# Kernel optimization log

Hardware: AMD Instinct MI355X
Metric: run time of the kernel (lower is better)

Reference implementation:

```python
import jax, jax.numpy as jnp
import numpy as np

C, H, W = 128, 128, 128
N_LINES = 8192
N_POINTS = 32
POOL = 4
DIM_FC = 1024


def setup_inputs() -> dict:
    key = jax.random.key(0)
    ks = jax.random.split(key, 8)
    feats = jax.random.normal(ks[0], (C, H, W), dtype=jnp.float32)
    # line endpoints (x1,y1,x2,y2) in feature-map pixel coords
    lines = jax.random.uniform(ks[1], (N_LINES, 4), dtype=jnp.float32) * (H - 1)
    d_in = C * (N_POINTS // POOL)  # 1024
    W1 = jax.random.normal(ks[2], (DIM_FC, d_in), dtype=jnp.float32) * 0.02
    b1 = jax.random.normal(ks[3], (DIM_FC,), dtype=jnp.float32) * 0.02
    W2 = jax.random.normal(ks[4], (DIM_FC, DIM_FC), dtype=jnp.float32) * 0.02
    b2 = jax.random.normal(ks[5], (DIM_FC,), dtype=jnp.float32) * 0.02
    W3 = jax.random.normal(ks[6], (4, DIM_FC), dtype=jnp.float32) * 0.02
    b3 = jax.random.normal(ks[7], (4,), dtype=jnp.float32) * 0.02
    return {
        "features_per_image": feats,
        "lines_per_im": lines,
        "W1": W1, "b1": b1, "W2": W2, "b2": b2, "W3": W3, "b3": b3,
        "n_points": N_POINTS,
        "pool_stride": POOL,
    }


def _extract_pt_feats(features, lines, n_points):
    # features: [C, H, W]; lines: [N, 4]
    c, h, w = features.shape
    tspan = jnp.linspace(0.0, 1.0, n_points).astype(features.dtype)  # [P]
    U, V = lines[:, :2], lines[:, 2:]
    # [N, 2, P] -> interpolate endpoints, shift by 0.5 (torch pixel-center convention)
    pts = U[:, :, None] * tspan + V[:, :, None] * (1.0 - tspan) - 0.5
    pts = pts.transpose(0, 2, 1).reshape(-1, 2)  # [N*P, 2]
    px, py = pts[:, 0], pts[:, 1]
    # NOTE: faithful to torch source: px indexes the h-axis but is clamped with w-1,
    # py indexes the w-axis but is clamped with h-1 (harmless here since H == W).
    px0 = jnp.clip(jnp.floor(px), 0.0, w - 1)
    py0 = jnp.clip(jnp.floor(py), 0.0, h - 1)
    px1 = jnp.clip(px0 + 1.0, 0.0, w - 1)
    py1 = jnp.clip(py0 + 1.0, 0.0, h - 1)
    px0i, py0i = px0.astype(jnp.int32), py0.astype(jnp.int32)
    px1i, py1i = px1.astype(jnp.int32), py1.astype(jnp.int32)
    # four irregular gathers + bilinear weights, fused expression. each term: [C, N*P]
    xp = (features[:, px0i, py0i] * ((py1 - py) * (px1 - px))
          + features[:, px0i, py1i] * ((py - py0) * (px1 - px))
          + features[:, px1i, py0i] * ((py1 - py) * (px - px0))
          + features[:, px1i, py1i] * ((py - py0) * (px - px0)))
    return xp.reshape(c, -1, n_points).transpose(1, 0, 2)  # [N, C, P]


def reference(features_per_image, lines_per_im, W1, b1, W2, b2, W3, b3,
              n_points, pool_stride):
    xp = _extract_pt_feats(features_per_image, lines_per_im, n_points)  # [N, C, P]
    n, c, p = xp.shape
    # MaxPool1d(kernel=stride=pool_stride)
    pooled = xp.reshape(n, c, p // pool_stride, pool_stride).max(axis=-1)
    flat = pooled.reshape(n, -1)  # [N, C*(P//s)]
    h1 = jax.nn.relu(flat @ W1.T + b1)
    h2 = jax.nn.relu(h1 @ W2.T + b2)
    return h2 @ W3.T + b3  # [N, 4]
```

## Files before the change

### kernel.cpp

```cpp
#include <hip/hip_runtime.h>
#include <hip/hip_bf16.h>
#include <cstdint>

typedef __attribute__((ext_vector_type(4))) float f32x4;
typedef __attribute__((ext_vector_type(8))) short short8;

#define DEVI __device__ __forceinline__

DEVI uint16_t f2bf(float v) {
    union { float f; uint32_t u; } c; c.f = v;
    uint32_t u = c.u + 0x7FFFu + ((c.u >> 16) & 1u);
    return (uint16_t)(u >> 16);
}
DEVI float bflo(uint32_t u) { union { uint32_t u; float f; } c; c.u = u << 16; return c.f; }
DEVI float bfhi(uint32_t u) { union { uint32_t u; float f; } c; c.u = u & 0xFFFF0000u; return c.f; }

DEVI void async16(const uint16_t* g, uint16_t* l) {
    __builtin_amdgcn_global_load_lds((const __attribute__((address_space(1))) void*)g,
                                     (__attribute__((address_space(3))) void*)l, 16, 0, 0);
}

__global__ __launch_bounds__(256) void init_out(float* __restrict__ out, const float* __restrict__ b3) {
    const int i = blockIdx.x * 256 + threadIdx.x;
    float4 b = { b3[0], b3[1], b3[2], b3[3] };
    ((float4*)out)[i] = b;
}

__global__ __launch_bounds__(256) void prep_all(const float* __restrict__ f, uint16_t* __restrict__ featT,
                                                const float* __restrict__ W1, uint16_t* __restrict__ W1b,
                                                const float* __restrict__ W2, uint16_t* __restrict__ W2b) {
    if (blockIdx.x < 128) {
        __shared__ uint16_t s[128 * 130];
        const int x = blockIdx.x;
        const float* fx = f + x * 128;
        for (int i = threadIdx.x; i < 16384; i += 256) {
            int c = i >> 7, y = i & 127;
            s[y * 130 + c] = f2bf(fx[c * 16384 + y]);
        }
        __syncthreads();
        uint16_t* o = featT + x * 16384;
        for (int i = threadIdx.x; i < 16384; i += 256) {
            int y = i >> 7, c = i & 127;
            o[i] = s[y * 130 + c];
        }
    } else {
        const int i = (blockIdx.x - 128) * 256 + threadIdx.x;
        float4 a = ((const float4*)W1)[i];
        float4 b = ((const float4*)W2)[i];
        ushort4 pa = { f2bf(a.x), f2bf(a.y), f2bf(a.z), f2bf(a.w) };
        ushort4 pb = { f2bf(b.x), f2bf(b.y), f2bf(b.z), f2bf(b.w) };
        ((ushort4*)W1b)[i] = pa;
        ((ushort4*)W2b)[i] = pb;
    }
}

__global__ __launch_bounds__(256) void extract_k(const float4* __restrict__ lines,
                                                 const uint16_t* __restrict__ featT,
                                                 uint16_t* __restrict__ flat) {
    const int n = blockIdx.x;
    const int tid = threadIdx.x;
    const int lane = tid & 63, wave = tid >> 6;
    const float4 ln = lines[n];
    __shared__ uint16_t ps[1024];
    const uint16_t* fb = featT + lane * 2;

    for (int g2 = 0; g2 < 2; ++g2) {
        const int g = wave * 2 + g2;
        float m0 = -1e30f, m1 = -1e30f;
#pragma unroll
        for (int pp = 0; pp < 4; ++pp) {
            const float t = (float)(g * 4 + pp) * (1.0f / 31.0f);
            const float x = ln.x * t + ln.z * (1.0f - t) - 0.5f;
            const float y = ln.y * t + ln.w * (1.0f - t) - 0.5f;
            const float x0f = fminf(fmaxf(floorf(x), 0.0f), 127.0f);
            const float y0f = fminf(fmaxf(floorf(y), 0.0f), 127.0f);
            const float x1f = fminf(x0f + 1.0f, 127.0f);
            const float y1f = fminf(y0f + 1.0f, 127.0f);
            const int x0 = (int)x0f, x1 = (int)x1f, y0 = (int)y0f, y1 = (int)y1f;
            const float wx1 = x - x0f, wx0 = x1f - x;
            const float wy1 = y - y0f, wy0 = y1f - y;
            const uint32_t u00 = *(const uint32_t*)(fb + ((x0 * 128 + y0) << 7));
            const uint32_t u01 = *(const uint32_t*)(fb + ((x0 * 128 + y1) << 7));
            const uint32_t u10 = *(const uint32_t*)(fb + ((x1 * 128 + y0) << 7));
            const uint32_t u11 = *(const uint32_t*)(fb + ((x1 * 128 + y1) << 7));
            const float w00 = wy0 * wx0, w01 = wy1 * wx0, w10 = wy0 * wx1, w11 = wy1 * wx1;
            const float a = bflo(u00) * w00 + bflo(u01) * w01 + bflo(u10) * w10 + bflo(u11) * w11;
            const float b = bfhi(u00) * w00 + bfhi(u01) * w01 + bfhi(u10) * w10 + bfhi(u11) * w11;
            m0 = fmaxf(m0, a);
            m1 = fmaxf(m1, b);
        }
        ps[lane * 16 + g]     = f2bf(m0);
        ps[lane * 16 + 8 + g] = f2bf(m1);
    }
    __syncthreads();
    *(uint2*)(flat + (size_t)n * 1024 + tid * 4) = ((const uint2*)ps)[tid];
}

template <int FUSE3>
__global__ __launch_bounds__(256) void gemm_bt(const uint16_t* __restrict__ A,
                                               const uint16_t* __restrict__ B,
                                               const float* __restrict__ bias,
                                               uint16_t* __restrict__ Co,
                                               const float* __restrict__ W3,
                                               float* __restrict__ out3,
                                               int M, int N, int K) {
    __shared__ uint16_t As[128 * 64];
    __shared__ uint16_t Bs[128 * 64];
    const int tid = threadIdx.x;
    const int lane = tid & 63, wave = tid >> 6;
    const int nbm = M >> 7;
    const int bm = blockIdx.x % nbm;
    const int bn = blockIdx.x / nbm;
    const int wr = wave >> 1, wc = wave & 1;
    const int l15 = lane & 15, l16 = lane >> 4;

    f32x4 acc[4][4] = {};

    const uint16_t* Ag = A + (size_t)(bm * 128) * K;
    const uint16_t* Bg = B + (size_t)(bn * 128) * K;

    for (int kt = 0; kt < K; kt += 64) {
        if (kt) __syncthreads();
#pragma unroll
        for (int i = 0; i < 4; ++i) {
            const int c = i * 256 + tid;
            const int row = c >> 3, slot = c & 7;
            const int s2 = slot ^ (row & 7);
            async16(Ag + (size_t)row * K + kt + s2 * 8, &As[c * 8]);
            async16(Bg + (size_t)row * K + kt + s2 * 8, &Bs[c * 8]);
        }
        __syncthreads();
        short8 a[4][2], b[4][2];
#pragma unroll
        for (int fm = 0; fm < 4; ++fm) {
            const int r = wr * 64 + fm * 16 + l15;
#pragma unroll
            for (int kk = 0; kk < 2; ++kk) {
                const int s2 = (kk * 4 + l16) ^ (r & 7);
                a[fm][kk] = *(const short8*)&As[r * 64 + s2 * 8];
            }
        }
#pragma unroll
        for (int fn = 0; fn < 4; ++fn) {
            const int r = wc * 64 + fn * 16 + l15;
#pragma unroll
            for (int kk = 0; kk < 2; ++kk) {
                const int s2 = (kk * 4 + l16) ^ (r & 7);
                b[fn][kk] = *(const short8*)&Bs[r * 64 + s2 * 8];
            }
        }
#pragma unroll
        for (int kk = 0; kk < 2; ++kk)
#pragma unroll
            for (int fm = 0; fm < 4; ++fm)
#pragma unroll
                for (int fn = 0; fn < 4; ++fn)
                    acc[fm][fn] = __builtin_amdgcn_mfma_f32_16x16x32_bf16(a[fm][kk], b[fn][kk], acc[fm][fn], 0, 0, 0);
    }

    if (!FUSE3) {
#pragma unroll
        for (int fm = 0; fm < 4; ++fm) {
            const int row = bm * 128 + wr * 64 + fm * 16 + l16 * 4;
#pragma unroll
            for (int fn = 0; fn < 4; ++fn) {
                const int col = bn * 128 + wc * 64 + fn * 16 + l15;
                const float bv = bias[col];
#pragma unroll
                for (int r = 0; r < 4; ++r) {
                    float v = fmaxf(acc[fm][fn][r] + bv, 0.0f);
                    Co[(size_t)(row + r) * N + col] = f2bf(v);
                }
            }
        }
    } else {
        float bv[4], w3v[4][4];
#pragma unroll
        for (int fn = 0; fn < 4; ++fn) {
            const int col = bn * 128 + wc * 64 + fn * 16 + l15;
            bv[fn] = bias[col];
#pragma unroll
            for (int j = 0; j < 4; ++j) w3v[j][fn] = W3[j * N + col];
        }
#pragma unroll
        for (int fm = 0; fm < 4; ++fm) {
            const int row = bm * 128 + wr * 64 + fm * 16 + l16 * 4;
#pragma unroll
            for (int r = 0; r < 4; ++r) {
                float p[4] = { 0.0f, 0.0f, 0.0f, 0.0f };
#pragma unroll
                for (int fn = 0; fn < 4; ++fn) {
                    const float hv = fmaxf(acc[fm][fn][r] + bv[fn], 0.0f);
#pragma unroll
                    for (int j = 0; j < 4; ++j) p[j] += hv * w3v[j][fn];
                }
#pragma unroll
                for (int off = 1; off <= 8; off <<= 1)
#pragma unroll
                    for (int j = 0; j < 4; ++j) p[j] += __shfl_xor(p[j], off);
                if (l15 == 0) {
                    float* o = out3 + (size_t)(row + r) * 4;
#pragma unroll
                    for (int j = 0; j < 4; ++j) atomicAdd(o + j, p[j]);
                }
            }
        }
    }
}

extern "C" void kernel_launch(void* const* d_in, const int* in_sizes, int n_in,
                              void* d_out, int out_size, void* d_ws, size_t ws_size,
                              hipStream_t stream) {
    const float* feats = (const float*)d_in[0];
    const float* lines = (const float*)d_in[1];
    const float* W1 = (const float*)d_in[2];
    const float* b1 = (const float*)d_in[3];
    const float* W2 = (const float*)d_in[4];
    const float* b2 = (const float*)d_in[5];
    const float* W3 = (const float*)d_in[6];
    const float* b3 = (const float*)d_in[7];
    float* out = (float*)d_out;

    char* ws = (char*)d_ws;
    uint16_t* featT = (uint16_t*)(ws);
    uint16_t* W1b   = (uint16_t*)(ws + (4u << 20));
    uint16_t* W2b   = (uint16_t*)(ws + (6u << 20));
    uint16_t* flat  = (uint16_t*)(ws + (8u << 20));
    uint16_t* h1    = (uint16_t*)(ws + (24u << 20));

    init_out<<<32, 256, 0, stream>>>(out, b3);
    prep_all<<<1152, 256, 0, stream>>>(feats, featT, W1, W1b, W2, W2b);
    extract_k<<<8192, 256, 0, stream>>>((const float4*)lines, featT, flat);
    gemm_bt<0><<<512, 256, 0, stream>>>(flat, W1b, b1, h1, nullptr, nullptr, 8192, 1024, 1024);
    gemm_bt<1><<<512, 256, 0, stream>>>(h1, W2b, b2, nullptr, W3, out, 8192, 1024, 1024);
}
```

Measured before the change: 108.3 us.

## Double-buffer GEMM LDS tiles with 32-wide K steps to overlap loads

Splits the 64-wide K tile into two 32-wide ping-pong LDS buffers so the async global-to-LDS load of the next tile is issued before the MFMA work on the current one. This is meant to hide global load latency behind compute. It drops the XOR swizzle on the LDS layout, which may introduce bank conflicts on the fragment reads, and it doubles the number of barriers per K.

```diff
diff --git a/kernel.cpp b/kernel.cpp
--- a/kernel.cpp
+++ b/kernel.cpp
@@ -96,6 +96,18 @@
     *(uint2*)(flat + (size_t)n * 1024 + tid * 4) = ((const uint2*)ps)[tid];
 }
 
+
+DEVI void stage_tile(const uint16_t* Ag, const uint16_t* Bg, int K, int kt,
+                     uint16_t* as, uint16_t* bs, int tid) {
+#pragma unroll
+    for (int i = 0; i < 2; ++i) {
+        const int c = i * 256 + tid;
+        const int row = c >> 2, off = (c & 3) * 8;
+        async16(Ag + (size_t)row * K + kt + off, as + c * 8);
+        async16(Bg + (size_t)row * K + kt + off, bs + c * 8);
+    }
+}
+
 template <int FUSE3>
 __global__ __launch_bounds__(256) void gemm_bt(const uint16_t* __restrict__ A,
                                                const uint16_t* __restrict__ B,
@@ -104,8 +116,10 @@
                                                const float* __restrict__ W3,
                                                float* __restrict__ out3,
                                                int M, int N, int K) {
-    __shared__ uint16_t As[128 * 64];
-    __shared__ uint16_t Bs[128 * 64];
+    __shared__ uint16_t As0[128 * 32];
+    __shared__ uint16_t Bs0[128 * 32];
+    __shared__ uint16_t As1[128 * 32];
+    __shared__ uint16_t Bs1[128 * 32];
     const int tid = threadIdx.x;
     const int lane = tid & 63, wave = tid >> 6;
     const int nbm = M >> 7;
@@ -119,44 +133,38 @@
     const uint16_t* Ag = A + (size_t)(bm * 128) * K;
     const uint16_t* Bg = B + (size_t)(bn * 128) * K;
 
-    for (int kt = 0; kt < K; kt += 64) {
-        if (kt) __syncthreads();
-#pragma unroll
-        for (int i = 0; i < 4; ++i) {
-            const int c = i * 256 + tid;
-            const int row = c >> 3, slot = c & 7;
-            const int s2 = slot ^ (row & 7);
-            async16(Ag + (size_t)row * K + kt + s2 * 8, &As[c * 8]);
-            async16(Bg + (size_t)row * K + kt + s2 * 8, &Bs[c * 8]);
-        }
+#define COMPUTE(asrc, bsrc)                                                          \
+    {                                                                                \
+        short8 a[4], b[4];                                                           \
+        _Pragma("unroll")                                                            \
+        for (int fm = 0; fm < 4; ++fm)                                               \
+            a[fm] = *(const short8*)&asrc[(wr * 64 + fm * 16 + l15) * 32 + l16 * 8]; \
+        _Pragma("unroll")                                                            \
+        for (int fn = 0; fn < 4; ++fn)                                               \
+            b[fn] = *(const short8*)&bsrc[(wc * 64 + fn * 16 + l15) * 32 + l16 * 8]; \
+        _Pragma("unroll")                                                            \
+        for (int fm = 0; fm < 4; ++fm)                                               \
+            _Pragma("unroll")                                                        \
+            for (int fn = 0; fn < 4; ++fn)                                           \
+                acc[fm][fn] = __builtin_amdgcn_mfma_f32_16x16x32_bf16(a[fm], b[fn], acc[fm][fn], 0, 0, 0); \
+    }
+
+    stage_tile(Ag, Bg, K, 0, As0, Bs0, tid);
+    __syncthreads();
+    int kt = 0;
+    for (; kt + 64 < K; kt += 64) {
+        stage_tile(Ag, Bg, K, kt + 32, As1, Bs1, tid);
+        COMPUTE(As0, Bs0);
         __syncthreads();
-        short8 a[4][2], b[4][2];
-#pragma unroll
-        for (int fm = 0; fm < 4; ++fm) {
-            const int r = wr * 64 + fm * 16 + l15;
-#pragma unroll
-            for (int kk = 0; kk < 2; ++kk) {
-                const int s2 = (kk * 4 + l16) ^ (r & 7);
-                a[fm][kk] = *(const short8*)&As[r * 64 + s2 * 8];
-            }
-        }
-#pragma unroll
-        for (int fn = 0; fn < 4; ++fn) {
-            const int r = wc * 64 + fn * 16 + l15;
-#pragma unroll
-            for (int kk = 0; kk < 2; ++kk) {
-                const int s2 = (kk * 4 + l16) ^ (r & 7);
-                b[fn][kk] = *(const short8*)&Bs[r * 64 + s2 * 8];
-            }
-        }
-#pragma unroll
-        for (int kk = 0; kk < 2; ++kk)
-#pragma unroll
-            for (int fm = 0; fm < 4; ++fm)
-#pragma unroll
-                for (int fn = 0; fn < 4; ++fn)
-                    acc[fm][fn] = __builtin_amdgcn_mfma_f32_16x16x32_bf16(a[fm][kk], b[fn][kk], acc[fm][fn], 0, 0, 0);
-    }
+        stage_tile(Ag, Bg, K, kt + 64, As0, Bs0, tid);
+        COMPUTE(As1, Bs1);
+        __syncthreads();
+    }
+    stage_tile(Ag, Bg, K, kt + 32, As1, Bs1, tid);
+    COMPUTE(As0, Bs0);
+    __syncthreads();
+    COMPUTE(As1, Bs1);
+#undef COMPUTE
 
     if (!FUSE3) {
 #pragma unroll
```

Result: slower. 116.5 us (+7.5%).

## Shrink GEMM tiles to 64x128 with K-step 32 and one wave per column strip

Applied to the files above, without the earlier changes.

Changes the bf16 GEMM block tile from 128x128 with K-step 64 to 64x128 with K-step 32. Each wave now owns a 64x32 output slice instead of a 64x64 one, and the grid doubles to 1024 blocks. The XOR swizzle on the LDS layout is removed. The goal is more blocks in flight and fewer accumulator registers, for better occupancy across CUs. The cost is lower arithmetic intensity per LDS load, twice as many sync points per K, and possible LDS bank conflicts from the unswizzled reads.

```diff
diff --git a/kernel.cpp b/kernel.cpp
--- a/kernel.cpp
+++ b/kernel.cpp
@@ -104,67 +104,54 @@
                                                const float* __restrict__ W3,
                                                float* __restrict__ out3,
                                                int M, int N, int K) {
-    __shared__ uint16_t As[128 * 64];
-    __shared__ uint16_t Bs[128 * 64];
+    __shared__ uint16_t As[64 * 32];
+    __shared__ uint16_t Bs[128 * 32];
     const int tid = threadIdx.x;
     const int lane = tid & 63, wave = tid >> 6;
-    const int nbm = M >> 7;
+    const int nbm = M >> 6;
     const int bm = blockIdx.x % nbm;
     const int bn = blockIdx.x / nbm;
-    const int wr = wave >> 1, wc = wave & 1;
     const int l15 = lane & 15, l16 = lane >> 4;
 
-    f32x4 acc[4][4] = {};
-
-    const uint16_t* Ag = A + (size_t)(bm * 128) * K;
+    f32x4 acc[4][2] = {};
+
+    const uint16_t* Ag = A + (size_t)(bm * 64) * K;
     const uint16_t* Bg = B + (size_t)(bn * 128) * K;
 
-    for (int kt = 0; kt < K; kt += 64) {
+    for (int kt = 0; kt < K; kt += 32) {
         if (kt) __syncthreads();
-#pragma unroll
-        for (int i = 0; i < 4; ++i) {
-            const int c = i * 256 + tid;
-            const int row = c >> 3, slot = c & 7;
-            const int s2 = slot ^ (row & 7);
-            async16(Ag + (size_t)row * K + kt + s2 * 8, &As[c * 8]);
-            async16(Bg + (size_t)row * K + kt + s2 * 8, &Bs[c * 8]);
+        {
+            const int arow = tid >> 2, aoff = (tid & 3) * 8;
+            async16(Ag + (size_t)arow * K + kt + aoff, &As[tid * 8]);
+#pragma unroll
+            for (int i = 0; i < 2; ++i) {
+                const int c = i * 256 + tid;
+                const int row = c >> 2, off = (c & 3) * 8;
+                async16(Bg + (size_t)row * K + kt + off, &Bs[c * 8]);
+            }
         }
         __syncthreads();
-        short8 a[4][2], b[4][2];
+        short8 a[4], b[2];
+#pragma unroll
+        for (int fm = 0; fm < 4; ++fm)
+            a[fm] = *(const short8*)&As[(fm * 16 + l15) * 32 + l16 * 8];
+#pragma unroll
+        for (int fn = 0; fn < 2; ++fn)
+            b[fn] = *(const short8*)&Bs[(wave * 32 + fn * 16 + l15) * 32 + l16 * 8];
+#pragma unroll
+        for (int fm = 0; fm < 4; ++fm)
+#pragma unroll
+            for (int fn = 0; fn < 2; ++fn)
+                acc[fm][fn] = __builtin_amdgcn_mfma_f32_16x16x32_bf16(a[fm], b[fn], acc[fm][fn], 0, 0, 0);
+    }
+
+    if (!FUSE3) {
 #pragma unroll
         for (int fm = 0; fm < 4; ++fm) {
-            const int r = wr * 64 + fm * 16 + l15;
-#pragma unroll
-            for (int kk = 0; kk < 2; ++kk) {
-                const int s2 = (kk * 4 + l16) ^ (r & 7);
-                a[fm][kk] = *(const short8*)&As[r * 64 + s2 * 8];
-            }
-        }
-#pragma unroll
-        for (int fn = 0; fn < 4; ++fn) {
-            const int r = wc * 64 + fn * 16 + l15;
-#pragma unroll
-            for (int kk = 0; kk < 2; ++kk) {
-                const int s2 = (kk * 4 + l16) ^ (r & 7);
-                b[fn][kk] = *(const short8*)&Bs[r * 64 + s2 * 8];
-            }
-        }
-#pragma unroll
-        for (int kk = 0; kk < 2; ++kk)
-#pragma unroll
-            for (int fm = 0; fm < 4; ++fm)
-#pragma unroll
-                for (int fn = 0; fn < 4; ++fn)
-                    acc[fm][fn] = __builtin_amdgcn_mfma_f32_16x16x32_bf16(a[fm][kk], b[fn][kk], acc[fm][fn], 0, 0, 0);
-    }
-
-    if (!FUSE3) {
-#pragma unroll
-        for (int fm = 0; fm < 4; ++fm) {
-            const int row = bm * 128 + wr * 64 + fm * 16 + l16 * 4;
-#pragma unroll
-            for (int fn = 0; fn < 4; ++fn) {
-                const int col = bn * 128 + wc * 64 + fn * 16 + l15;
+            const int row = bm * 64 + fm * 16 + l16 * 4;
+#pragma unroll
+            for (int fn = 0; fn < 2; ++fn) {
+                const int col = bn * 128 + wave * 32 + fn * 16 + l15;
                 const float bv = bias[col];
 #pragma unroll
                 for (int r = 0; r < 4; ++r) {
@@ -174,22 +161,22 @@
             }
         }
     } else {
-        float bv[4], w3v[4][4];
-#pragma unroll
-        for (int fn = 0; fn < 4; ++fn) {
-            const int col = bn * 128 + wc * 64 + fn * 16 + l15;
+        float bv[2], w3v[4][2];
+#pragma unroll
+        for (int fn = 0; fn < 2; ++fn) {
+            const int col = bn * 128 + wave * 32 + fn * 16 + l15;
             bv[fn] = bias[col];
 #pragma unroll
             for (int j = 0; j < 4; ++j) w3v[j][fn] = W3[j * N + col];
         }
 #pragma unroll
         for (int fm = 0; fm < 4; ++fm) {
-            const int row = bm * 128 + wr * 64 + fm * 16 + l16 * 4;
+            const int row = bm * 64 + fm * 16 + l16 * 4;
 #pragma unroll
             for (int r = 0; r < 4; ++r) {
                 float p[4] = { 0.0f, 0.0f, 0.0f, 0.0f };
 #pragma unroll
-                for (int fn = 0; fn < 4; ++fn) {
+                for (int fn = 0; fn < 2; ++fn) {
                     const float hv = fmaxf(acc[fm][fn][r] + bv[fn], 0.0f);
 #pragma unroll
                     for (int j = 0; j < 4; ++j) p[j] += hv * w3v[j][fn];
@@ -231,6 +218,6 @@
     init_out<<<32, 256, 0, stream>>>(out, b3);
     prep_all<<<1152, 256, 0, stream>>>(feats, featT, W1, W1b, W2, W2b);
     extract_k<<<8192, 256, 0, stream>>>((const float4*)lines, featT, flat);
-    gemm_bt<0><<<512, 256, 0, stream>>>(flat, W1b, b1, h1, nullptr, nullptr, 8192, 1024, 1024);
-    gemm_bt<1><<<512, 256, 0, stream>>>(h1, W2b, b2, nullptr, W3, out, 8192, 1024, 1024);
-}
+    gemm_bt<0><<<1024, 256, 0, stream>>>(flat, W1b, b1, h1, nullptr, nullptr, 8192, 1024, 1024);
+    gemm_bt<1><<<1024, 256, 0, stream>>>(h1, W2b, b2, nullptr, W3, out, 8192, 1024, 1024);
+}
```

Measured after the change: 166.8 us. 1.54x slower.
